# Optimization experiments

Hardware: AMD Instinct MI355X
Metric: run time of the kernel (lower is better)

Reference implementation:

```python
import jax, jax.numpy as jnp
import numpy as np

B, N, NPOINT, NSAMPLE = 8, 8192, 512, 32
D, NHEAD, NLAYERS, DIM_OUT = 128, 8, 4, 256
HD = D // NHEAD
DFF = 2 * D
EPS = 1e-5

_gather = jax.vmap(lambda p, i: p[i])  # p: [N,C], i: [...] -> [...,C]


def _ln(x, g, b):
    m = jnp.mean(x, -1, keepdims=True)
    v = jnp.var(x, -1, keepdims=True)
    return (x - m) / jnp.sqrt(v + EPS) * g + b


def _fps(pts):
    # pts: [B,N,3] -> centroid indices [B,NPOINT]; start index 0 (torch uses randint)
    Bb, Nn, _ = pts.shape
    def step(carry, _):
        dist, far = carry
        cen = jax.vmap(lambda p, f: p[f])(pts, far)[:, None, :]  # [B,1,3]
        dist = jnp.minimum(dist, jnp.sum((pts - cen) ** 2, -1))
        return (dist, jnp.argmax(dist, -1)), far
    init = (jnp.full((Bb, Nn), 1e10, pts.dtype), jnp.zeros((Bb,), jnp.int32))
    _, cents = jax.lax.scan(step, init, None, length=NPOINT)
    return cents.T  # [B,NPOINT]


def _interp_linear(x, n_out):
    # x: [B,C,S] -> [B,C,n_out], linear, align_corners=True
    S = x.shape[-1]
    pos = jnp.arange(n_out) * ((S - 1) / (n_out - 1))
    i0 = jnp.floor(pos).astype(jnp.int32)
    i1 = jnp.minimum(i0 + 1, S - 1)
    w = (pos - i0).astype(x.dtype)
    return x[..., i0] * (1 - w) + x[..., i1] * w


def _layer(x, p):
    wqkv, bqkv, wo, bo, g1, be1, w1, bf1, w2, bf2, g2, be2 = p
    Bt, K, _ = x.shape
    qkv = x @ wqkv.T + bqkv
    q, k, v = jnp.split(qkv, 3, axis=-1)
    q = q.reshape(Bt, K, NHEAD, HD)
    k = k.reshape(Bt, K, NHEAD, HD)
    v = v.reshape(Bt, K, NHEAD, HD)
    att = jax.nn.softmax(jnp.einsum('bqhd,bkhd->bhqk', q, k) / jnp.sqrt(jnp.float32(HD)), axis=-1)
    o = jnp.einsum('bhqk,bkhd->bqhd', att, v).reshape(Bt, K, D)
    x = _ln(x + o @ wo.T + bo, g1, be1)
    ff = jax.nn.relu(x @ w1.T + bf1) @ w2.T + bf2
    return _ln(x + ff, g2, be2)


def setup_inputs():
    key = jax.random.key(0)
    ks = jax.random.split(key, 10)
    w = lambda k, s: jax.random.normal(k, s, jnp.float32) * 0.02
    return {
        'xyz': jax.random.normal(ks[0], (B, 3, N), jnp.float32),
        'features': jax.random.normal(ks[1], (B, D, N), jnp.float32),
        'pe_w1': w(ks[2], (D // 2, 3)), 'pe_b1': jnp.zeros((D // 2,), jnp.float32),
        'bn_gamma': jnp.ones((D // 2,), jnp.float32), 'bn_beta': jnp.zeros((D // 2,), jnp.float32),
        'bn_mean': jnp.zeros((D // 2,), jnp.float32), 'bn_var': jnp.ones((D // 2,), jnp.float32),
        'pe_w2': w(ks[3], (D, D // 2)), 'pe_b2': jnp.zeros((D,), jnp.float32),
        'attn_wqkv': w(ks[4], (NLAYERS, 3 * D, D)), 'attn_bqkv': jnp.zeros((NLAYERS, 3 * D), jnp.float32),
        'attn_wo': w(ks[5], (NLAYERS, D, D)), 'attn_bo': jnp.zeros((NLAYERS, D), jnp.float32),
        'ln1_g': jnp.ones((NLAYERS, D), jnp.float32), 'ln1_b': jnp.zeros((NLAYERS, D), jnp.float32),
        'ffn_w1': w(ks[6], (NLAYERS, DFF, D)), 'ffn_b1': jnp.zeros((NLAYERS, DFF), jnp.float32),
        'ffn_w2': w(ks[7], (NLAYERS, D, DFF)), 'ffn_b2': jnp.zeros((NLAYERS, D), jnp.float32),
        'ln2_g': jnp.ones((NLAYERS, D), jnp.float32), 'ln2_b': jnp.zeros((NLAYERS, D), jnp.float32),
        'fc_w': w(ks[8], (DIM_OUT, D)), 'fc_b': jnp.zeros((DIM_OUT,), jnp.float32),
    }


def reference(xyz, features, pe_w1, pe_b1, bn_gamma, bn_beta, bn_mean, bn_var, pe_w2, pe_b2,
              attn_wqkv, attn_bqkv, attn_wo, attn_bo, ln1_g, ln1_b,
              ffn_w1, ffn_b1, ffn_w2, ffn_b2, ln2_g, ln2_b, fc_w, fc_b):
    pts = jnp.transpose(xyz, (0, 2, 1))                 # [B,N,3]
    fps_idx = _fps(pts)                                 # [B,S]
    new_xyz = _gather(pts, fps_idx)                     # [B,S,3]
    # kNN: squared distances [B,S,N]
    d2 = (jnp.sum(new_xyz ** 2, -1)[..., None] + jnp.sum(pts ** 2, -1)[:, None, :]
          - 2.0 * jnp.einsum('bsc,bnc->bsn', new_xyz, pts))
    _, gidx = jax.lax.top_k(-d2, NSAMPLE)               # [B,S,K]
    gxyz = _gather(pts, gidx)                           # [B,S,K,3]
    gfeat = _gather(jnp.transpose(features, (0, 2, 1)), gidx)  # [B,S,K,D]
    # positional encoding: 1x1 conv -> BN (eval) -> relu -> 1x1 conv
    h = gxyz @ pe_w1.T + pe_b1
    h = (h - bn_mean) / jnp.sqrt(bn_var + EPS) * bn_gamma + bn_beta
    pe = jax.nn.relu(h) @ pe_w2.T + pe_b2               # [B,S,K,D]
    x = (gfeat + pe).reshape(B * NPOINT, NSAMPLE, D)    # tokens: K neighbors per center
    layer_params = (attn_wqkv, attn_bqkv, attn_wo, attn_bo, ln1_g, ln1_b,
                    ffn_w1, ffn_b1, ffn_w2, ffn_b2, ln2_g, ln2_b)
    x, _ = jax.lax.scan(lambda c, p: (_layer(c, p), None), x, layer_params)
    x = x.reshape(B, NPOINT, NSAMPLE, D).max(axis=2)    # max-pool over neighbors [B,S,D]
    out = jnp.transpose(x @ fc_w.T + fc_b, (0, 2, 1))   # [B,DIM_OUT,S]
    out_up = _interp_linear(out, N)                     # [B,DIM_OUT,N]
    return jnp.transpose(new_xyz, (0, 2, 1)), out_up
```

## Files before the change

### kernel.cpp

```cpp
#include <hip/hip_runtime.h>
#include <math.h>

constexpr int CB  = 8;
constexpr int CN  = 8192;
constexpr int CS  = 512;
constexpr int CK  = 32;
constexpr int CD  = 128;
constexpr int CF  = 256;
constexpr int CO  = 256;
constexpr float CEPS = 1e-5f;

typedef __attribute__((ext_vector_type(8)))  short short8;
typedef __attribute__((ext_vector_type(4)))  float f32x4;
typedef __attribute__((ext_vector_type(16))) float f32x16;
#define MFMA16(a,b,c) __builtin_amdgcn_mfma_f32_16x16x32_bf16(a,b,c,0,0,0)
#define MFMA32(a,b,c) __builtin_amdgcn_mfma_f32_32x32x16_bf16(a,b,c,0,0,0)

__device__ __forceinline__ ushort f2b(float f){
  unsigned u = __builtin_bit_cast(unsigned, f);
  u = u + 0x7fffu + ((u >> 16) & 1u);
  return (ushort)(u >> 16);
}

template<int CTRL, int RM>
__device__ __forceinline__ unsigned long long dpp64(unsigned long long k){
  int lo = (int)(unsigned)k;
  int hi = (int)(unsigned)(k >> 32);
  int plo = __builtin_amdgcn_update_dpp(lo, lo, CTRL, RM, 0xF, false);
  int phi = __builtin_amdgcn_update_dpp(hi, hi, CTRL, RM, 0xF, false);
  return ((unsigned long long)(unsigned)phi << 32) | (unsigned)plo;
}
__device__ __forceinline__ unsigned long long wave_max64(unsigned long long k){
  unsigned long long p;
  p = dpp64<0xB1,0xF>(k); k = p > k ? p : k;
  p = dpp64<0x4E,0xF>(k); k = p > k ? p : k;
  p = dpp64<0x140,0xF>(k); k = p > k ? p : k;
  p = dpp64<0x141,0xF>(k); k = p > k ? p : k;
  p = dpp64<0x142,0xA>(k); k = p > k ? p : k;
  p = dpp64<0x143,0xC>(k); k = p > k ? p : k;
  return k;
}
__device__ __forceinline__ unsigned long long wave_min64(unsigned long long k){
  unsigned long long p;
  p = dpp64<0xB1,0xF>(k); k = p < k ? p : k;
  p = dpp64<0x4E,0xF>(k); k = p < k ? p : k;
  p = dpp64<0x140,0xF>(k); k = p < k ? p : k;
  p = dpp64<0x141,0xF>(k); k = p < k ? p : k;
  p = dpp64<0x142,0xA>(k); k = p < k ? p : k;
  p = dpp64<0x143,0xC>(k); k = p < k ? p : k;
  return k;
}
__device__ __forceinline__ unsigned long long oct_max64(unsigned long long k){
  unsigned long long p;
  p = dpp64<0xB1,0xF>(k); k = p > k ? p : k;
  p = dpp64<0x4E,0xF>(k); k = p > k ? p : k;
  p = dpp64<0x141,0xF>(k); k = p > k ? p : k;
  return k;
}
__device__ __forceinline__ unsigned long long quad_min64(unsigned long long k){
  unsigned long long p;
  p = dpp64<0xB1,0xF>(k); k = p < k ? p : k;
  p = dpp64<0x4E,0xF>(k); k = p < k ? p : k;
  return k;
}

__global__ __launch_bounds__(512)
void fps_kernel(const float* __restrict__ xyz, int* __restrict__ fps_idx)
{
#pragma clang fp contract(off)
  __shared__ __align__(16) float4 p4[CN];
  __shared__ unsigned long long wred[2][8];
  const int b = blockIdx.x, t = threadIdx.x;
  const int w = t >> 6, lane = t & 63;
  const float* xb = xyz + (size_t)b*3*CN;
  float px[16], py[16], pz[16], dist[16];
  #pragma unroll
  for (int j=0;j<16;j++){
    const int i = t + 512*j;
    px[j] = xb[i]; py[j] = xb[CN+i]; pz[j] = xb[2*CN+i];
    dist[j] = 1e10f;
    p4[i] = make_float4(px[j], py[j], pz[j], 0.f);
  }
  __syncthreads();
  int far = 0, par = 0;
  float4 c = p4[0];
  for (int it = 0; it < CS; ++it){
    if (t == 0) fps_idx[b*CS + it] = far;
    unsigned long long kk[16];
    #pragma unroll
    for (int j=0;j<16;j++){
      const float dx = px[j]-c.x, dy = py[j]-c.y, dz = pz[j]-c.z;
      const float d2 = (dx*dx + dy*dy) + dz*dz;
      const float nd = fminf(dist[j], d2);
      dist[j] = nd;
      kk[j] = ((unsigned long long)__builtin_bit_cast(unsigned, nd) << 32)
              | (unsigned)(8191 - (t + 512*j));
    }
    #pragma unroll
    for (int st=1; st<16; st<<=1)
      #pragma unroll
      for (int j=0;j<16;j+=2*st)
        kk[j] = kk[j] >= kk[j+st] ? kk[j] : kk[j+st];
    unsigned long long key = wave_max64(kk[0]);
    key = __shfl(key, 63);
    if (lane == 0) wred[par][w] = key;
    __syncthreads();
    unsigned long long k2 = wred[par][lane & 7];
    k2 = oct_max64(k2);
    far = 8191 - (int)(k2 & 0xFFFFFFFFu);
    c = p4[far];
    par ^= 1;
  }
}

__global__ __launch_bounds__(256)
void knn_kernel(const float* __restrict__ xyz, const int* __restrict__ fps_idx,
                int* __restrict__ gidx)
{
#pragma clang fp contract(off)
  __shared__ unsigned long long wredk[2][4];
  const int blk = blockIdx.x, t = threadIdx.x;
  const int w = t >> 6, l = t & 63;
  const int b = blk >> 9;
  const int s = blk & 511;
  const float* xb = xyz + (size_t)b*3*CN;
  const int cidx = fps_idx[b*CS + s];
  const float cx = xb[cidx], cy = xb[CN+cidx], cz = xb[2*CN+cidx];
  const float cn2 = (cx*cx + cy*cy) + cz*cz;
  unsigned long long kv[32];
  #pragma unroll
  for (int j=0;j<32;j++){
    const int i = t + 256*j;
    const float x = xb[i], y = xb[CN+i], z = xb[2*CN+i];
    const float pn2 = (x*x + y*y) + z*z;
    const float dot = (cx*x + cy*y) + cz*z;
    const float d2 = (cn2 + pn2) - 2.0f*dot;
    unsigned u = __builtin_bit_cast(unsigned, d2);
    u ^= (unsigned)((int)u >> 31) | 0x80000000u;
    kv[j] = ((unsigned long long)u << 32) | (unsigned)i;
  }
  unsigned long long mv;
  {
    unsigned long long tmp[16];
    #pragma unroll
    for (int j=0;j<16;j++) tmp[j] = kv[j] < kv[j+16] ? kv[j] : kv[j+16];
    #pragma unroll
    for (int st=8; st>=1; st>>=1)
      #pragma unroll
      for (int j=0;j<st;j++) tmp[j] = tmp[j] < tmp[j+st] ? tmp[j] : tmp[j+st];
    mv = tmp[0];
  }
  int par = 0;
  for (int k=0;k<CK;k++){
    unsigned long long v = wave_min64(mv);
    v = __shfl(v, 63);
    if (l == 0) wredk[par][w] = v;
    __syncthreads();
    unsigned long long k2 = wredk[par][l & 3];
    k2 = quad_min64(k2);
    const int win = (int)(k2 & 0xFFFFFFFFu);
    if (t == 0) gidx[(size_t)blk*CK + k] = win;
    if ((win & 255) == t){
      const int jw = win >> 8;
      #pragma unroll
      for (int j=0;j<32;j++) if (j == jw) kv[j] = ~0ull;
      unsigned long long tmp[16];
      #pragma unroll
      for (int j=0;j<16;j++) tmp[j] = kv[j] < kv[j+16] ? kv[j] : kv[j+16];
      #pragma unroll
      for (int st=8; st>=1; st>>=1)
        #pragma unroll
        for (int j=0;j<st;j++) tmp[j] = tmp[j] < tmp[j+st] ? tmp[j] : tmp[j+st];
      mv = tmp[0];
    }
    par ^= 1;
  }
}

__global__ __launch_bounds__(256)
void newxyz_kernel(const float* __restrict__ xyz, const int* __restrict__ fps_idx,
                   float* __restrict__ out0)
{
  const int idx = blockIdx.x*256 + threadIdx.x;
  if (idx >= CB*3*CS) return;
  const int s = idx & 511;
  const int c = (idx >> 9) % 3;
  const int b = idx / (3*CS);
  const int n = fps_idx[b*CS + s];
  out0[idx] = xyz[(size_t)b*3*CN + (size_t)c*CN + n];
}

__global__ __launch_bounds__(256)
void transpose_kernel(const float* __restrict__ f, float* __restrict__ ft)
{
  __shared__ float tile[32][33];
  const int b = blockIdx.z, d0 = blockIdx.y*32, n0 = blockIdx.x*32;
  const int tx = threadIdx.x, ty = threadIdx.y;
  const float* fb = f + (size_t)b*CD*CN;
  #pragma unroll
  for (int r=0;r<32;r+=8) tile[ty+r][tx] = fb[(size_t)(d0+ty+r)*CN + n0+tx];
  __syncthreads();
  float* ftb = ft + (size_t)b*CN*CD;
  #pragma unroll
  for (int r=0;r<32;r+=8) ftb[(size_t)(n0+ty+r)*CD + d0+tx] = tile[tx][ty+r];
}

__global__ __launch_bounds__(256)
void pe_kernel(const float* __restrict__ xyz, const float* __restrict__ features,
               const float* __restrict__ featT, const int* __restrict__ gidx,
               const float* __restrict__ pe_w1, const float* __restrict__ pe_b1,
               const float* __restrict__ bn_g, const float* __restrict__ bn_b,
               const float* __restrict__ bn_m, const float* __restrict__ bn_v,
               const float* __restrict__ pe_w2, const float* __restrict__ pe_b2,
               float* __restrict__ xout)
{
  __shared__ __align__(16) float w2s[CD*68];
  __shared__ __align__(16) float hr[CK*68];
  __shared__ int idxs[CK];
  __shared__ float gx[CK], gy[CK], gz[CK];
  const int g = blockIdx.x, t = threadIdx.x;
  const int b = g >> 9;
  for (int i=t; i<CD*64; i+=256) w2s[(i>>6)*68 + (i&63)] = pe_w2[i];
  if (t < CK){
    const int id = gidx[(size_t)g*CK + t];
    idxs[t] = id;
    const float* xb = xyz + (size_t)b*3*CN;
    gx[t] = xb[id]; gy[t] = xb[CN+id]; gz[t] = xb[2*CN+id];
  }
  __syncthreads();
  for (int v=t; v<CK*64; v+=256){
    const int k = v>>6, j = v&63;
    float h = ((gx[k]*pe_w1[j*3] + gy[k]*pe_w1[j*3+1]) + gz[k]*pe_w1[j*3+2]) + pe_b1[j];
    h = (h - bn_m[j]) / sqrtf(bn_v[j] + CEPS) * bn_g[j] + bn_b[j];
    hr[k*68+j] = fmaxf(h, 0.f);
  }
  __syncthreads();
  const int kt = t >> 5, dt = t & 31;
  const int k0 = kt*4, d0 = dt*4;
  float acc[4][4];
  #pragma unroll
  for (int a=0;a<4;a++)
    #pragma unroll
    for (int bb=0;bb<4;bb++) acc[a][bb] = 0.f;
  for (int j=0;j<16;j++){
    float4 h4[4], w4[4];
    #pragma unroll
    for (int a=0;a<4;a++) h4[a] = *(const float4*)&hr[(k0+a)*68 + j*4];
    #pragma unroll
    for (int bb=0;bb<4;bb++) w4[bb] = *(const float4*)&w2s[(d0+bb)*68 + j*4];
    #pragma unroll
    for (int a=0;a<4;a++)
      #pragma unroll
      for (int bb=0;bb<4;bb++){
        acc[a][bb] += h4[a].x*w4[bb].x; acc[a][bb] += h4[a].y*w4[bb].y;
        acc[a][bb] += h4[a].z*w4[bb].z; acc[a][bb] += h4[a].w*w4[bb].w;
      }
  }
  const float4 b2v = *(const float4*)&pe_b2[d0];
  const float* fb  = features + (size_t)b*CD*CN;
  const float* ftb = featT ? (featT + (size_t)b*CN*CD) : nullptr;
  #pragma unroll
  for (int a=0;a<4;a++){
    const int id = idxs[k0+a];
    float4 gf;
    if (ftb) gf = *(const float4*)&ftb[(size_t)id*CD + d0];
    else gf = make_float4(fb[(size_t)(d0+0)*CN+id], fb[(size_t)(d0+1)*CN+id],
                          fb[(size_t)(d0+2)*CN+id], fb[(size_t)(d0+3)*CN+id]);
    float4 o;
    o.x = gf.x + (acc[a][0] + b2v.x);
    o.y = gf.y + (acc[a][1] + b2v.y);
    o.z = gf.z + (acc[a][2] + b2v.z);
    o.w = gf.w + (acc[a][3] + b2v.w);
    *(float4*)&xout[(size_t)g*4096 + (size_t)(k0+a)*128 + d0] = o;
  }
}

__global__ __launch_bounds__(256)
void wprep_kernel(const float* __restrict__ wqkv, const float* __restrict__ wo,
                  const float* __restrict__ w1,   const float* __restrict__ w2,
                  ushort* __restrict__ dst)
{
  const int tid = blockIdx.x*256 + threadIdx.x;
  const int l = tid & 63;
  const int f = tid >> 6;
  const int L = f >> 8;
  const int r = f & 255;
  const float* src; int stride, nt, kt;
  if (r < 96)      { nt = r>>2;        kt = r&3;        src = wqkv + (size_t)L*384*128; stride = 128; }
  else if (r < 128){ nt = (r-96)>>2;   kt = (r-96)&3;   src = wo   + (size_t)L*128*128; stride = 128; }
  else if (r < 192){ nt = (r-128)>>2;  kt = (r-128)&3;  src = w1   + (size_t)L*256*128; stride = 128; }
  else             { nt = (r-192)>>3;  kt = (r-192)&7;  src = w2   + (size_t)L*128*256; stride = 256; }
  const int n = nt*16 + (l & 15);
  const int k = kt*32 + (l >> 4)*8;
  const float* p = src + (size_t)n*stride + k;
  uint4 o;
  o.x = (unsigned)f2b(p[0]) | ((unsigned)f2b(p[1])<<16);
  o.y = (unsigned)f2b(p[2]) | ((unsigned)f2b(p[3])<<16);
  o.z = (unsigned)f2b(p[4]) | ((unsigned)f2b(p[5])<<16);
  o.w = (unsigned)f2b(p[6]) | ((unsigned)f2b(p[7])<<16);
  *(uint4*)(dst + (size_t)tid*8) = o;
}

__device__ __forceinline__ void ln_inplace(float* x32s, ushort* xbv,
                                           const float* __restrict__ gamma,
                                           const float* __restrict__ beta, int t)
{
  const int r = t >> 3, j = t & 7;
  float v[16]; float s = 0.f;
  #pragma unroll
  for (int i=0;i<16;i++){ v[i] = x32s[r*132 + j + 8*i]; s += v[i]; }
  #pragma unroll
  for (int off=1; off<8; off<<=1) s += __shfl_xor(s, off);
  const float mean = s * (1.f/128.f);
  float var = 0.f;
  #pragma unroll
  for (int i=0;i<16;i++){ const float d = v[i]-mean; var += d*d; }
  #pragma unroll
  for (int off=1; off<8; off<<=1) var += __shfl_xor(var, off);
  const float inv = 1.f / sqrtf(var*(1.f/128.f) + CEPS);
  #pragma unroll
  for (int i=0;i<16;i++){
    const int d = j + 8*i;
    const float o = (v[i]-mean)*inv*gamma[d] + beta[d];
    x32s[r*132 + d] = o;
    xbv[r*136 + d] = f2b(o);
  }
}

__global__ __launch_bounds__(256, 2)
void layer_mfma_kernel(float* __restrict__ xbuf, const ushort* __restrict__ wf,
                       const float* __restrict__ bqkv, const float* __restrict__ bo,
                       const float* __restrict__ g1, const float* __restrict__ b1v,
                       const float* __restrict__ bf1, const float* __restrict__ bf2,
                       const float* __restrict__ g2, const float* __restrict__ b2v)
{
  __shared__ __align__(16) float  x32s[32*132];
  __shared__ __align__(16) ushort xbv [32*136];
  __shared__ __align__(16) ushort qk  [32*264];
  __shared__ __align__(16) ushort vT  [128*40];
  __shared__ __align__(16) ushort Pb  [4*32*40];
  const int g = blockIdx.x, t = threadIdx.x;
  const int w = t>>6, l = t&63;
  const int l15 = l&15, q4 = l>>4, l31 = l&31, hi = l>>5;
  float* xg = xbuf + (size_t)g*1024*4;
  const uint4* wfv = (const uint4*)wf;

  for (int i=t;i<1024;i+=256){
    const float4 v = ((const float4*)xg)[i];
    const int r = i>>5, c = (i&31)*4;
    *(float4*)&x32s[r*132 + c] = v;
    uint2 p;
    p.x = (unsigned)f2b(v.x) | ((unsigned)f2b(v.y)<<16);
    p.y = (unsigned)f2b(v.z) | ((unsigned)f2b(v.w)<<16);
    *(uint2*)&xbv[r*136 + c] = p;
  }
  __syncthreads();

  {
    short8 a[2][4];
    #pragma unroll
    for (int mt=0;mt<2;mt++)
      #pragma unroll
      for (int kt=0;kt<4;kt++)
        a[mt][kt] = __builtin_bit_cast(short8, *(const uint4*)&xbv[(l15+16*mt)*136 + kt*32 + q4*8]);
    for (int i=0;i<6;i++){
      const int nt = w + 4*i;
      const int n  = nt*16 + l15;
      f32x4 a0 = {0.f,0.f,0.f,0.f}, a1 = {0.f,0.f,0.f,0.f};
      #pragma unroll
      for (int kt=0;kt<4;kt++){
        const short8 b = __builtin_bit_cast(short8, wfv[(nt*4+kt)*64 + l]);
        a0 = MFMA16(a[0][kt], b, a0);
        a1 = MFMA16(a[1][kt], b, a1);
      }
      const float bias = bqkv[n];
      if (nt < 16){
        #pragma unroll
        for (int i2=0;i2<4;i2++){
          qk[(q4*4+i2   )*264 + n] = f2b(a0[i2]+bias);
          qk[(q4*4+i2+16)*264 + n] = f2b(a1[i2]+bias);
        }
      } else {
        const int d = n - 256;
        uint2 p0, p1;
        p0.x = (unsigned)f2b(a0[0]+bias) | ((unsigned)f2b(a0[1]+bias)<<16);
        p0.y = (unsigned)f2b(a0[2]+bias) | ((unsigned)f2b(a0[3]+bias)<<16);
        p1.x = (unsigned)f2b(a1[0]+bias) | ((unsigned)f2b(a1[1]+bias)<<16);
        p1.y = (unsigned)f2b(a1[2]+bias) | ((unsigned)f2b(a1[3]+bias)<<16);
        *(uint2*)&vT[d*40 + q4*4]      = p0;
        *(uint2*)&vT[d*40 + 16 + q4*4] = p1;
      }
    }
  }
  __syncthreads();

  for (int hh=0; hh<2; hh++){
    const int h = 2*w + hh;
    const short8 ka = __builtin_bit_cast(short8, *(const uint4*)&qk[l31*264 + 128 + h*16 + hi*8]);
    const short8 qb = __builtin_bit_cast(short8, *(const uint4*)&qk[l31*264 +       h*16 + hi*8]);
    f32x16 s;
    #pragma unroll
    for (int i=0;i<16;i++) s[i] = 0.f;
    s = MFMA32(ka, qb, s);
    float e[16]; float mx = -1e30f;
    #pragma unroll
    for (int i=0;i<16;i++){ e[i] = s[i]*0.25f; mx = fmaxf(mx, e[i]); }
    mx = fmaxf(mx, __shfl_xor(mx, 32));
    float sum = 0.f;
    #pragma unroll
    for (int i=0;i<16;i++){ e[i] = __expf(e[i]-mx); sum += e[i]; }
    sum += __shfl_xor(sum, 32);
    const float inv = 1.f/sum;
    #pragma unroll
    for (int j=0;j<4;j++){
      uint2 p;
      p.x = (unsigned)f2b(e[4*j  ]*inv) | ((unsigned)f2b(e[4*j+1]*inv)<<16);
      p.y = (unsigned)f2b(e[4*j+2]*inv) | ((unsigned)f2b(e[4*j+3]*inv)<<16);
      *(uint2*)&Pb[w*1280 + l31*40 + j*8 + hi*4] = p;
    }
    const short8 bv = __builtin_bit_cast(short8, *(const uint4*)&vT[(h*16+l15)*40 + q4*8]);
    #pragma unroll
    for (int mt=0;mt<2;mt++){
      const short8 ap = __builtin_bit_cast(short8, *(const uint4*)&Pb[w*1280 + (l15+16*mt)*40 + q4*8]);
      f32x4 o = {0.f,0.f,0.f,0.f};
      o = MFMA16(ap, bv, o);
      #pragma unroll
      for (int i2=0;i2<4;i2++)
        xbv[(16*mt + q4*4 + i2)*136 + h*16 + l15] = f2b(o[i2]);
    }
  }
  __syncthreads();

  {
    short8 a[2][4];
    #pragma unroll
    for (int mt=0;mt<2;mt++)
      #pragma unroll
      for (int kt=0;kt<4;kt++)
        a[mt][kt] = __builtin_bit_cast(short8, *(const uint4*)&xbv[(l15+16*mt)*136 + kt*32 + q4*8]);
    for (int i=0;i<2;i++){
      const int nt = w + 4*i;
      const int n  = nt*16 + l15;
      f32x4 a0 = {0.f,0.f,0.f,0.f}, a1 = {0.f,0.f,0.f,0.f};
      #pragma unroll
      for (int kt=0;kt<4;kt++){
        const short8 b = __builtin_bit_cast(short8, wfv[(96 + nt*4+kt)*64 + l]);
        a0 = MFMA16(a[0][kt], b, a0);
        a1 = MFMA16(a[1][kt], b, a1);
      }
      const float bias = bo[n];
      #pragma unroll
      for (int i2=0;i2<4;i2++){
        x32s[(q4*4+i2   )*132 + n] += a0[i2] + bias;
        x32s[(q4*4+i2+16)*132 + n] += a1[i2] + bias;
      }
    }
  }
  __syncthreads();
  ln_inplace(x32s, xbv, g1, b1v, t);
  __syncthreads();

  {
    short8 a[2][4];
    #pragma unroll
    for (int mt=0;mt<2;mt++)
      #pragma unroll
      for (int kt=0;kt<4;kt++)
        a[mt][kt] = __builtin_bit_cast(short8, *(const uint4*)&xbv[(l15+16*mt)*136 + kt*32 + q4*8]);
    for (int i=0;i<4;i++){
      const int nt = w + 4*i;
      const int n  = nt*16 + l15;
      f32x4 a0 = {0.f,0.f,0.f,0.f}, a1 = {0.f,0.f,0.f,0.f};
      #pragma unroll
      for (int kt=0;kt<4;kt++){
        const short8 b = __builtin_bit_cast(short8, wfv[(128 + nt*4+kt)*64 + l]);
        a0 = MFMA16(a[0][kt], b, a0);
        a1 = MFMA16(a[1][kt], b, a1);
      }
      const float bias = bf1[n];
      #pragma unroll
      for (int i2=0;i2<4;i2++){
        qk[(q4*4+i2   )*264 + n] = f2b(fmaxf(a0[i2]+bias, 0.f));
        qk[(q4*4+i2+16)*264 + n] = f2b(fmaxf(a1[i2]+bias, 0.f));
      }
    }
  }
  __syncthreads();

  {
    short8 a[2][8];
    #pragma unroll
    for (int mt=0;mt<2;mt++)
      #pragma unroll
      for (int kt=0;kt<8;kt++)
        a[mt][kt] = __builtin_bit_cast(short8, *(const uint4*)&qk[(l15+16*mt)*264 + kt*32 + q4*8]);
    for (int i=0;i<2;i++){
      const int nt = w + 4*i;
      const int n  = nt*16 + l15;
      f32x4 a0 = {0.f,0.f,0.f,0.f}, a1 = {0.f,0.f,0.f,0.f};
      #pragma unroll
      for (int kt=0;kt<8;kt++){
        const short8 b = __builtin_bit_cast(short8, wfv[(192 + nt*8+kt)*64 + l]);
        a0 = MFMA16(a[0][kt], b, a0);
        a1 = MFMA16(a[1][kt], b, a1);
      }
      const float bias = bf2[n];
      #pragma unroll
      for (int i2=0;i2<4;i2++){
        x32s[(q4*4+i2   )*132 + n] += a0[i2] + bias;
        x32s[(q4*4+i2+16)*132 + n] += a1[i2] + bias;
      }
    }
  }
  __syncthreads();
  ln_inplace(x32s, xbv, g2, b2v, t);
  __syncthreads();

  for (int i=t;i<1024;i+=256){
    const int r = i>>5, c = (i&31)*4;
    ((float4*)xg)[i] = *(const float4*)&x32s[r*132 + c];
  }
}

__global__ __launch_bounds__(256)
void poolfc_kernel(const float* __restrict__ xbuf, const float* __restrict__ fc_w,
                   const float* __restrict__ fc_b, float* __restrict__ fcout)
{
  __shared__ __align__(16) float pooled[CD];
  const int gg = blockIdx.x, t = threadIdx.x;
  const float* xg = xbuf + (size_t)gg*CK*CD;
  if (t < CD){
    float m = -1e30f;
    for (int k=0;k<CK;k++) m = fmaxf(m, xg[(size_t)k*CD + t]);
    pooled[t] = m;
  }
  __syncthreads();
  const float* wr = fc_w + (size_t)t*CD;
  float acc = 0.f;
  const float4* pp = (const float4*)pooled;
  for (int i=0;i<CD/4;i++){
    const float4 w4 = *(const float4*)(wr + 4*i);
    const float4 p4 = pp[i];
    acc += p4.x*w4.x; acc += p4.y*w4.y; acc += p4.z*w4.z; acc += p4.w*w4.w;
  }
  acc += fc_b[t];
  const int b = gg >> 9, s = gg & 511;
  fcout[((size_t)b*CS + s)*CO + t] = acc;
}

__global__ __launch_bounds__(256)
void interp_kernel(const float* __restrict__ fcout, float* __restrict__ out1)
{
  const int idx = blockIdx.x*256 + threadIdx.x;
  const int n  = idx & (CN-1);
  const int bo = idx >> 13;
  const int b  = bo >> 8, o = bo & 255;
  const double pos = (double)n * ((double)(CS-1)/(double)(CN-1));
  const int i0 = (int)pos;
  const int i1 = min(i0+1, CS-1);
  const float w = (float)(pos - (double)i0);
  const float v0 = fcout[((size_t)b*CS + i0)*CO + o];
  const float v1 = fcout[((size_t)b*CS + i1)*CO + o];
  out1[idx] = v0*(1.f - w) + v1*w;
}

extern "C" void kernel_launch(void* const* d_in, const int* in_sizes, int n_in,
                              void* d_out, int out_size, void* d_ws, size_t ws_size,
                              hipStream_t stream)
{
  (void)in_sizes; (void)n_in; (void)out_size;
  const float* xyz      = (const float*)d_in[0];
  const float* features = (const float*)d_in[1];
  const float* pe_w1    = (const float*)d_in[2];
  const float* pe_b1    = (const float*)d_in[3];
  const float* bn_g     = (const float*)d_in[4];
  const float* bn_b     = (const float*)d_in[5];
  const float* bn_m     = (const float*)d_in[6];
  const float* bn_v     = (const float*)d_in[7];
  const float* pe_w2    = (const float*)d_in[8];
  const float* pe_b2    = (const float*)d_in[9];
  const float* wqkv     = (const float*)d_in[10];
  const float* bqkv     = (const float*)d_in[11];
  const float* wo       = (const float*)d_in[12];
  const float* bo       = (const float*)d_in[13];
  const float* g1       = (const float*)d_in[14];
  const float* b1       = (const float*)d_in[15];
  const float* w1       = (const float*)d_in[16];
  const float* bf1      = (const float*)d_in[17];
  const float* w2       = (const float*)d_in[18];
  const float* bf2      = (const float*)d_in[19];
  const float* g2       = (const float*)d_in[20];
  const float* b2       = (const float*)d_in[21];
  const float* fc_w     = (const float*)d_in[22];
  const float* fc_b     = (const float*)d_in[23];

  char* ws = (char*)d_ws;
  int*    fps_idx = (int*)(ws);
  int*    gidx    = (int*)(ws + (16u<<10));
  ushort* wfrag   = (ushort*)(ws + (1u<<20));
  float*  xbuf    = (float*)(ws + (2u<<20));
  float*  fcout   = (float*)(ws + (66u<<20));
  float*  featT   = (float*)(ws + (70u<<20));
  const bool useT = ws_size >= ((size_t)102<<20);

  float* out0 = (float*)d_out;
  float* out1 = out0 + CB*3*CS;

  fps_kernel<<<CB, 512, 0, stream>>>(xyz, fps_idx);
  knn_kernel<<<CB*CS, 256, 0, stream>>>(xyz, fps_idx, gidx);
  newxyz_kernel<<<(CB*3*CS + 255)/256, 256, 0, stream>>>(xyz, fps_idx, out0);
  wprep_kernel<<<256, 256, 0, stream>>>(wqkv, wo, w1, w2, wfrag);
  if (useT){
    dim3 tb(32, 8), tg(CN/32, CD/32, CB);
    transpose_kernel<<<tg, tb, 0, stream>>>(features, featT);
  }
  pe_kernel<<<CB*CS, 256, 0, stream>>>(xyz, features, useT ? featT : nullptr, gidx,
                                       pe_w1, pe_b1, bn_g, bn_b, bn_m, bn_v,
                                       pe_w2, pe_b2, xbuf);
  for (int L=0; L<4; L++){
    layer_mfma_kernel<<<CB*CS, 256, 0, stream>>>(xbuf,
        wfrag + (size_t)L*131072,
        bqkv + (size_t)L*3*CD, bo + (size_t)L*CD,
        g1 + (size_t)L*CD, b1 + (size_t)L*CD,
        bf1 + (size_t)L*CF, bf2 + (size_t)L*CD,
        g2 + (size_t)L*CD, b2 + (size_t)L*CD);
  }
  poolfc_kernel<<<CB*CS, 256, 0, stream>>>(xbuf, fc_w, fc_b, fcout);
  interp_kernel<<<(CB*CO*CN)/256, 256, 0, stream>>>(fcout, out1);
}
```

Baseline: 1.456 ms.

## Fuse transformer layers and pooling into one kernel, overlap prep work with FPS

Runs all four transformer layers plus max-pool and the FC projection inside a single kernel that keeps the 32x128 token tile in shared memory, removing the per-layer global round trips of xbuf and several launches. The weight fragment preparation and the feature transpose become extra blocks of the FPS launch, so they run on otherwise idle CUs while the 8-block FPS executes. The new_xyz output is now written by the KNN kernel, and the wave reductions drop a shuffle by storing from lane 63. In exchange, the FPS launch is larger and shares its shared-memory allocation with the transpose blocks.

```diff
diff --git a/kernel.cpp b/kernel.cpp
--- a/kernel.cpp
+++ b/kernel.cpp
@@ -65,12 +65,60 @@
 }
 
 __global__ __launch_bounds__(512)
-void fps_kernel(const float* __restrict__ xyz, int* __restrict__ fps_idx)
+void fps_fused_kernel(const float* __restrict__ xyz, int* __restrict__ fps_idx,
+                      const float* __restrict__ features, float* __restrict__ featT,
+                      const float* __restrict__ wqkv, const float* __restrict__ wo,
+                      const float* __restrict__ w1,   const float* __restrict__ w2,
+                      ushort* __restrict__ wfrag)
 {
 #pragma clang fp contract(off)
   __shared__ __align__(16) float4 p4[CN];
   __shared__ unsigned long long wred[2][8];
-  const int b = blockIdx.x, t = threadIdx.x;
+  const int bid = blockIdx.x, t = threadIdx.x;
+
+  if (bid >= CB + 128){
+    if (featT == nullptr) return;
+    const int tt  = (bid - CB - 128)*2 + (t >> 8);
+    const int b2  = tt >> 10;
+    const int rem = tt & 1023;
+    const int d0  = (rem >> 8) * 32;
+    const int n0  = (rem & 255) * 32;
+    const int t2  = t & 255;
+    const int tx  = t2 & 31, ty = t2 >> 5;
+    float* tl = ((float*)p4) + (t >> 8) * (32*33);
+    const float* fb = features + (size_t)b2*CD*CN;
+    #pragma unroll
+    for (int r=0;r<32;r+=8) tl[(ty+r)*33 + tx] = fb[(size_t)(d0+ty+r)*CN + n0+tx];
+    __syncthreads();
+    float* ftb = featT + (size_t)b2*CN*CD;
+    #pragma unroll
+    for (int r=0;r<32;r+=8) ftb[(size_t)(n0+ty+r)*CD + d0+tx] = tl[tx*33 + (ty+r)];
+    return;
+  }
+  if (bid >= CB){
+    const int tid = (bid - CB)*512 + t;
+    const int l = tid & 63;
+    const int f = tid >> 6;
+    const int L = f >> 8;
+    const int r = f & 255;
+    const float* src; int stride, nt, kt;
+    if (r < 96)      { nt = r>>2;        kt = r&3;        src = wqkv + (size_t)L*384*128; stride = 128; }
+    else if (r < 128){ nt = (r-96)>>2;   kt = (r-96)&3;   src = wo   + (size_t)L*128*128; stride = 128; }
+    else if (r < 192){ nt = (r-128)>>2;  kt = (r-128)&3;  src = w1   + (size_t)L*256*128; stride = 128; }
+    else             { nt = (r-192)>>3;  kt = (r-192)&7;  src = w2   + (size_t)L*128*256; stride = 256; }
+    const int n = nt*16 + (l & 15);
+    const int k = kt*32 + (l >> 4)*8;
+    const float* p = src + (size_t)n*stride + k;
+    uint4 o;
+    o.x = (unsigned)f2b(p[0]) | ((unsigned)f2b(p[1])<<16);
+    o.y = (unsigned)f2b(p[2]) | ((unsigned)f2b(p[3])<<16);
+    o.z = (unsigned)f2b(p[4]) | ((unsigned)f2b(p[5])<<16);
+    o.w = (unsigned)f2b(p[6]) | ((unsigned)f2b(p[7])<<16);
+    *(uint4*)(wfrag + (size_t)tid*8) = o;
+    return;
+  }
+
+  const int b = bid;
   const int w = t >> 6, lane = t & 63;
   const float* xb = xyz + (size_t)b*3*CN;
   float px[16], py[16], pz[16], dist[16];
@@ -101,9 +149,8 @@
       #pragma unroll
       for (int j=0;j<16;j+=2*st)
         kk[j] = kk[j] >= kk[j+st] ? kk[j] : kk[j+st];
-    unsigned long long key = wave_max64(kk[0]);
-    key = __shfl(key, 63);
-    if (lane == 0) wred[par][w] = key;
+    const unsigned long long key = wave_max64(kk[0]);
+    if (lane == 63) wred[par][w] = key;
     __syncthreads();
     unsigned long long k2 = wred[par][lane & 7];
     k2 = oct_max64(k2);
@@ -115,7 +162,7 @@
 
 __global__ __launch_bounds__(256)
 void knn_kernel(const float* __restrict__ xyz, const int* __restrict__ fps_idx,
-                int* __restrict__ gidx)
+                int* __restrict__ gidx, float* __restrict__ out0)
 {
 #pragma clang fp contract(off)
   __shared__ unsigned long long wredk[2][4];
@@ -127,6 +174,10 @@
   const int cidx = fps_idx[b*CS + s];
   const float cx = xb[cidx], cy = xb[CN+cidx], cz = xb[2*CN+cidx];
   const float cn2 = (cx*cx + cy*cy) + cz*cz;
+  if (t == 0){
+    float* o = out0 + (size_t)b*3*CS + s;
+    o[0] = cx; o[CS] = cy; o[2*CS] = cz;
+  }
   unsigned long long kv[32];
   #pragma unroll
   for (int j=0;j<32;j++){
@@ -152,9 +203,8 @@
   }
   int par = 0;
   for (int k=0;k<CK;k++){
-    unsigned long long v = wave_min64(mv);
-    v = __shfl(v, 63);
-    if (l == 0) wredk[par][w] = v;
+    const unsigned long long v = wave_min64(mv);
+    if (l == 63) wredk[par][w] = v;
     __syncthreads();
     unsigned long long k2 = wredk[par][l & 3];
     k2 = quad_min64(k2);
@@ -175,34 +225,6 @@
     }
     par ^= 1;
   }
-}
-
-__global__ __launch_bounds__(256)
-void newxyz_kernel(const float* __restrict__ xyz, const int* __restrict__ fps_idx,
-                   float* __restrict__ out0)
-{
-  const int idx = blockIdx.x*256 + threadIdx.x;
-  if (idx >= CB*3*CS) return;
-  const int s = idx & 511;
-  const int c = (idx >> 9) % 3;
-  const int b = idx / (3*CS);
-  const int n = fps_idx[b*CS + s];
-  out0[idx] = xyz[(size_t)b*3*CN + (size_t)c*CN + n];
-}
-
-__global__ __launch_bounds__(256)
-void transpose_kernel(const float* __restrict__ f, float* __restrict__ ft)
-{
-  __shared__ float tile[32][33];
-  const int b = blockIdx.z, d0 = blockIdx.y*32, n0 = blockIdx.x*32;
-  const int tx = threadIdx.x, ty = threadIdx.y;
-  const float* fb = f + (size_t)b*CD*CN;
-  #pragma unroll
-  for (int r=0;r<32;r+=8) tile[ty+r][tx] = fb[(size_t)(d0+ty+r)*CN + n0+tx];
-  __syncthreads();
-  float* ftb = ft + (size_t)b*CN*CD;
-  #pragma unroll
-  for (int r=0;r<32;r+=8) ftb[(size_t)(n0+ty+r)*CD + d0+tx] = tile[tx][ty+r];
 }
 
 __global__ __launch_bounds__(256)
@@ -275,32 +297,6 @@
   }
 }
 
-__global__ __launch_bounds__(256)
-void wprep_kernel(const float* __restrict__ wqkv, const float* __restrict__ wo,
-                  const float* __restrict__ w1,   const float* __restrict__ w2,
-                  ushort* __restrict__ dst)
-{
-  const int tid = blockIdx.x*256 + threadIdx.x;
-  const int l = tid & 63;
-  const int f = tid >> 6;
-  const int L = f >> 8;
-  const int r = f & 255;
-  const float* src; int stride, nt, kt;
-  if (r < 96)      { nt = r>>2;        kt = r&3;        src = wqkv + (size_t)L*384*128; stride = 128; }
-  else if (r < 128){ nt = (r-96)>>2;   kt = (r-96)&3;   src = wo   + (size_t)L*128*128; stride = 128; }
-  else if (r < 192){ nt = (r-128)>>2;  kt = (r-128)&3;  src = w1   + (size_t)L*256*128; stride = 128; }
-  else             { nt = (r-192)>>3;  kt = (r-192)&7;  src = w2   + (size_t)L*128*256; stride = 256; }
-  const int n = nt*16 + (l & 15);
-  const int k = kt*32 + (l >> 4)*8;
-  const float* p = src + (size_t)n*stride + k;
-  uint4 o;
-  o.x = (unsigned)f2b(p[0]) | ((unsigned)f2b(p[1])<<16);
-  o.y = (unsigned)f2b(p[2]) | ((unsigned)f2b(p[3])<<16);
-  o.z = (unsigned)f2b(p[4]) | ((unsigned)f2b(p[5])<<16);
-  o.w = (unsigned)f2b(p[6]) | ((unsigned)f2b(p[7])<<16);
-  *(uint4*)(dst + (size_t)tid*8) = o;
-}
-
 __device__ __forceinline__ void ln_inplace(float* x32s, ushort* xbv,
                                            const float* __restrict__ gamma,
                                            const float* __restrict__ beta, int t)
@@ -328,22 +324,24 @@
 }
 
 __global__ __launch_bounds__(256, 2)
-void layer_mfma_kernel(float* __restrict__ xbuf, const ushort* __restrict__ wf,
-                       const float* __restrict__ bqkv, const float* __restrict__ bo,
-                       const float* __restrict__ g1, const float* __restrict__ b1v,
-                       const float* __restrict__ bf1, const float* __restrict__ bf2,
-                       const float* __restrict__ g2, const float* __restrict__ b2v)
+void layers_mfma_kernel(const float* __restrict__ xbuf, const ushort* __restrict__ wf,
+                        const float* __restrict__ bqkv, const float* __restrict__ bo,
+                        const float* __restrict__ g1, const float* __restrict__ b1v,
+                        const float* __restrict__ bf1, const float* __restrict__ bf2,
+                        const float* __restrict__ g2, const float* __restrict__ b2v,
+                        const float* __restrict__ fc_w, const float* __restrict__ fc_b,
+                        float* __restrict__ fcout)
 {
   __shared__ __align__(16) float  x32s[32*132];
   __shared__ __align__(16) ushort xbv [32*136];
   __shared__ __align__(16) ushort qk  [32*264];
   __shared__ __align__(16) ushort vT  [128*40];
   __shared__ __align__(16) ushort Pb  [4*32*40];
+  __shared__ __align__(16) float  pooled[CD];
   const int g = blockIdx.x, t = threadIdx.x;
   const int w = t>>6, l = t&63;
   const int l15 = l&15, q4 = l>>4, l31 = l&31, hi = l>>5;
-  float* xg = xbuf + (size_t)g*1024*4;
-  const uint4* wfv = (const uint4*)wf;
+  const float* xg = xbuf + (size_t)g*1024*4;
 
   for (int i=t;i<1024;i+=256){
     const float4 v = ((const float4*)xg)[i];
@@ -356,196 +354,197 @@
   }
   __syncthreads();
 
-  {
-    short8 a[2][4];
-    #pragma unroll
-    for (int mt=0;mt<2;mt++)
-      #pragma unroll
-      for (int kt=0;kt<4;kt++)
-        a[mt][kt] = __builtin_bit_cast(short8, *(const uint4*)&xbv[(l15+16*mt)*136 + kt*32 + q4*8]);
-    for (int i=0;i<6;i++){
-      const int nt = w + 4*i;
-      const int n  = nt*16 + l15;
-      f32x4 a0 = {0.f,0.f,0.f,0.f}, a1 = {0.f,0.f,0.f,0.f};
-      #pragma unroll
-      for (int kt=0;kt<4;kt++){
-        const short8 b = __builtin_bit_cast(short8, wfv[(nt*4+kt)*64 + l]);
-        a0 = MFMA16(a[0][kt], b, a0);
-        a1 = MFMA16(a[1][kt], b, a1);
-      }
-      const float bias = bqkv[n];
-      if (nt < 16){
-        #pragma unroll
-        for (int i2=0;i2<4;i2++){
-          qk[(q4*4+i2   )*264 + n] = f2b(a0[i2]+bias);
-          qk[(q4*4+i2+16)*264 + n] = f2b(a1[i2]+bias);
-        }
-      } else {
-        const int d = n - 256;
-        uint2 p0, p1;
-        p0.x = (unsigned)f2b(a0[0]+bias) | ((unsigned)f2b(a0[1]+bias)<<16);
-        p0.y = (unsigned)f2b(a0[2]+bias) | ((unsigned)f2b(a0[3]+bias)<<16);
-        p1.x = (unsigned)f2b(a1[0]+bias) | ((unsigned)f2b(a1[1]+bias)<<16);
-        p1.y = (unsigned)f2b(a1[2]+bias) | ((unsigned)f2b(a1[3]+bias)<<16);
-        *(uint2*)&vT[d*40 + q4*4]      = p0;
-        *(uint2*)&vT[d*40 + 16 + q4*4] = p1;
+  #pragma unroll 1
+  for (int L = 0; L < 4; ++L){
+    const uint4*  wfv   = (const uint4*)(wf + (size_t)L*131072);
+    const float* bqkvL  = bqkv + (size_t)L*3*CD;
+    const float* boL    = bo   + (size_t)L*CD;
+    const float* g1L    = g1   + (size_t)L*CD;
+    const float* b1L    = b1v  + (size_t)L*CD;
+    const float* bf1L   = bf1  + (size_t)L*CF;
+    const float* bf2L   = bf2  + (size_t)L*CD;
+    const float* g2L    = g2   + (size_t)L*CD;
+    const float* b2L    = b2v  + (size_t)L*CD;
+
+    {
+      short8 a[2][4];
+      #pragma unroll
+      for (int mt=0;mt<2;mt++)
+        #pragma unroll
+        for (int kt=0;kt<4;kt++)
+          a[mt][kt] = __builtin_bit_cast(short8, *(const uint4*)&xbv[(l15+16*mt)*136 + kt*32 + q4*8]);
+      for (int i=0;i<6;i++){
+        const int nt = w + 4*i;
+        const int n  = nt*16 + l15;
+        f32x4 a0 = {0.f,0.f,0.f,0.f}, a1 = {0.f,0.f,0.f,0.f};
+        #pragma unroll
+        for (int kt=0;kt<4;kt++){
+          const short8 b = __builtin_bit_cast(short8, wfv[(nt*4+kt)*64 + l]);
+          a0 = MFMA16(a[0][kt], b, a0);
+          a1 = MFMA16(a[1][kt], b, a1);
+        }
+        const float bias = bqkvL[n];
+        if (nt < 16){
+          #pragma unroll
+          for (int i2=0;i2<4;i2++){
+            qk[(q4*4+i2   )*264 + n] = f2b(a0[i2]+bias);
+            qk[(q4*4+i2+16)*264 + n] = f2b(a1[i2]+bias);
+          }
+        } else {
+          const int d = n - 256;
+          uint2 p0, p1;
+          p0.x = (unsigned)f2b(a0[0]+bias) | ((unsigned)f2b(a0[1]+bias)<<16);
+          p0.y = (unsigned)f2b(a0[2]+bias) | ((unsigned)f2b(a0[3]+bias)<<16);
+          p1.x = (unsigned)f2b(a1[0]+bias) | ((unsigned)f2b(a1[1]+bias)<<16);
+          p1.y = (unsigned)f2b(a1[2]+bias) | ((unsigned)f2b(a1[3]+bias)<<16);
+          *(uint2*)&vT[d*40 + q4*4]      = p0;
+          *(uint2*)&vT[d*40 + 16 + q4*4] = p1;
+        }
       }
     }
-  }
-  __syncthreads();
-
-  for (int hh=0; hh<2; hh++){
-    const int h = 2*w + hh;
-    const short8 ka = __builtin_bit_cast(short8, *(const uint4*)&qk[l31*264 + 128 + h*16 + hi*8]);
-    const short8 qb = __builtin_bit_cast(short8, *(const uint4*)&qk[l31*264 +       h*16 + hi*8]);
-    f32x16 s;
-    #pragma unroll
-    for (int i=0;i<16;i++) s[i] = 0.f;
-    s = MFMA32(ka, qb, s);
-    float e[16]; float mx = -1e30f;
-    #pragma unroll
-    for (int i=0;i<16;i++){ e[i] = s[i]*0.25f; mx = fmaxf(mx, e[i]); }
-    mx = fmaxf(mx, __shfl_xor(mx, 32));
-    float sum = 0.f;
-    #pragma unroll
-    for (int i=0;i<16;i++){ e[i] = __expf(e[i]-mx); sum += e[i]; }
-    sum += __shfl_xor(sum, 32);
-    const float inv = 1.f/sum;
-    #pragma unroll
-    for (int j=0;j<4;j++){
-      uint2 p;
-      p.x = (unsigned)f2b(e[4*j  ]*inv) | ((unsigned)f2b(e[4*j+1]*inv)<<16);
-      p.y = (unsigned)f2b(e[4*j+2]*inv) | ((unsigned)f2b(e[4*j+3]*inv)<<16);
-      *(uint2*)&Pb[w*1280 + l31*40 + j*8 + hi*4] = p;
-    }
-    const short8 bv = __builtin_bit_cast(short8, *(const uint4*)&vT[(h*16+l15)*40 + q4*8]);
-    #pragma unroll
-    for (int mt=0;mt<2;mt++){
-      const short8 ap = __builtin_bit_cast(short8, *(const uint4*)&Pb[w*1280 + (l15+16*mt)*40 + q4*8]);
-      f32x4 o = {0.f,0.f,0.f,0.f};
-      o = MFMA16(ap, bv, o);
-      #pragma unroll
-      for (int i2=0;i2<4;i2++)
-        xbv[(16*mt + q4*4 + i2)*136 + h*16 + l15] = f2b(o[i2]);
-    }
-  }
-  __syncthreads();
-
-  {
-    short8 a[2][4];
-    #pragma unroll
-    for (int mt=0;mt<2;mt++)
-      #pragma unroll
-      for (int kt=0;kt<4;kt++)
-        a[mt][kt] = __builtin_bit_cast(short8, *(const uint4*)&xbv[(l15+16*mt)*136 + kt*32 + q4*8]);
-    for (int i=0;i<2;i++){
-      const int nt = w + 4*i;
-      const int n  = nt*16 + l15;
-      f32x4 a0 = {0.f,0.f,0.f,0.f}, a1 = {0.f,0.f,0.f,0.f};
-      #pragma unroll
-      for (int kt=0;kt<4;kt++){
-        const short8 b = __builtin_bit_cast(short8, wfv[(96 + nt*4+kt)*64 + l]);
-        a0 = MFMA16(a[0][kt], b, a0);
-        a1 = MFMA16(a[1][kt], b, a1);
+    __syncthreads();
+
+    for (int hh=0; hh<2; hh++){
+      const int h = 2*w + hh;
+      const short8 ka = __builtin_bit_cast(short8, *(const uint4*)&qk[l31*264 + 128 + h*16 + hi*8]);
+      const short8 qb = __builtin_bit_cast(short8, *(const uint4*)&qk[l31*264 +       h*16 + hi*8]);
+      f32x16 s;
+      #pragma unroll
+      for (int i=0;i<16;i++) s[i] = 0.f;
+      s = MFMA32(ka, qb, s);
+      float e[16]; float mx = -1e30f;
+      #pragma unroll
+      for (int i=0;i<16;i++){ e[i] = s[i]*0.25f; mx = fmaxf(mx, e[i]); }
+      mx = fmaxf(mx, __shfl_xor(mx, 32));
+      float sum = 0.f;
+      #pragma unroll
+      for (int i=0;i<16;i++){ e[i] = __expf(e[i]-mx); sum += e[i]; }
+      sum += __shfl_xor(sum, 32);
+      const float inv = 1.f/sum;
+      #pragma unroll
+      for (int j=0;j<4;j++){
+        uint2 p;
+        p.x = (unsigned)f2b(e[4*j  ]*inv) | ((unsigned)f2b(e[4*j+1]*inv)<<16);
+        p.y = (unsigned)f2b(e[4*j+2]*inv) | ((unsigned)f2b(e[4*j+3]*inv)<<16);
+        *(uint2*)&Pb[w*1280 + l31*40 + j*8 + hi*4] = p;
       }
-      const float bias = bo[n];
-      #pragma unroll
-      for (int i2=0;i2<4;i2++){
-        x32s[(q4*4+i2   )*132 + n] += a0[i2] + bias;
-        x32s[(q4*4+i2+16)*132 + n] += a1[i2] + bias;
+      const short8 bv = __builtin_bit_cast(short8, *(const uint4*)&vT[(h*16+l15)*40 + q4*8]);
+      #pragma unroll
+      for (int mt=0;mt<2;mt++){
+        const short8 ap = __builtin_bit_cast(short8, *(const uint4*)&Pb[w*1280 + (l15+16*mt)*40 + q4*8]);
+        f32x4 o = {0.f,0.f,0.f,0.f};
+        o = MFMA16(ap, bv, o);
+        #pragma unroll
+        for (int i2=0;i2<4;i2++)
+          xbv[(16*mt + q4*4 + i2)*136 + h*16 + l15] = f2b(o[i2]);
       }
     }
-  }
-  __syncthreads();
-  ln_inplace(x32s, xbv, g1, b1v, t);
-  __syncthreads();
-
-  {
-    short8 a[2][4];
-    #pragma unroll
-    for (int mt=0;mt<2;mt++)
-      #pragma unroll
-      for (int kt=0;kt<4;kt++)
-        a[mt][kt] = __builtin_bit_cast(short8, *(const uint4*)&xbv[(l15+16*mt)*136 + kt*32 + q4*8]);
-    for (int i=0;i<4;i++){
-      const int nt = w + 4*i;
-      const int n  = nt*16 + l15;
-      f32x4 a0 = {0.f,0.f,0.f,0.f}, a1 = {0.f,0.f,0.f,0.f};
-      #pragma unroll
-      for (int kt=0;kt<4;kt++){
-        const short8 b = __builtin_bit_cast(short8, wfv[(128 + nt*4+kt)*64 + l]);
-        a0 = MFMA16(a[0][kt], b, a0);
-        a1 = MFMA16(a[1][kt], b, a1);
-      }
-      const float bias = bf1[n];
-      #pragma unroll
-      for (int i2=0;i2<4;i2++){
-        qk[(q4*4+i2   )*264 + n] = f2b(fmaxf(a0[i2]+bias, 0.f));
-        qk[(q4*4+i2+16)*264 + n] = f2b(fmaxf(a1[i2]+bias, 0.f));
+    __syncthreads();
+
+    {
+      short8 a[2][4];
+      #pragma unroll
+      for (int mt=0;mt<2;mt++)
+        #pragma unroll
+        for (int kt=0;kt<4;kt++)
+          a[mt][kt] = __builtin_bit_cast(short8, *(const uint4*)&xbv[(l15+16*mt)*136 + kt*32 + q4*8]);
+      for (int i=0;i<2;i++){
+        const int nt = w + 4*i;
+        const int n  = nt*16 + l15;
+        f32x4 a0 = {0.f,0.f,0.f,0.f}, a1 = {0.f,0.f,0.f,0.f};
+        #pragma unroll
+        for (int kt=0;kt<4;kt++){
+          const short8 b = __builtin_bit_cast(short8, wfv[(96 + nt*4+kt)*64 + l]);
+          a0 = MFMA16(a[0][kt], b, a0);
+          a1 = MFMA16(a[1][kt], b, a1);
+        }
+        const float bias = boL[n];
+        #pragma unroll
+        for (int i2=0;i2<4;i2++){
+          x32s[(q4*4+i2   )*132 + n] += a0[i2] + bias;
+          x32s[(q4*4+i2+16)*132 + n] += a1[i2] + bias;
+        }
       }
     }
-  }
-  __syncthreads();
-
-  {
-    short8 a[2][8];
-    #pragma unroll
-    for (int mt=0;mt<2;mt++)
-      #pragma unroll
-      for (int kt=0;kt<8;kt++)
-        a[mt][kt] = __builtin_bit_cast(short8, *(const uint4*)&qk[(l15+16*mt)*264 + kt*32 + q4*8]);
-    for (int i=0;i<2;i++){
-      const int nt = w + 4*i;
-      const int n  = nt*16 + l15;
-      f32x4 a0 = {0.f,0.f,0.f,0.f}, a1 = {0.f,0.f,0.f,0.f};
-      #pragma unroll
-      for (int kt=0;kt<8;kt++){
-        const short8 b = __builtin_bit_cast(short8, wfv[(192 + nt*8+kt)*64 + l]);
-        a0 = MFMA16(a[0][kt], b, a0);
-        a1 = MFMA16(a[1][kt], b, a1);
-      }
-      const float bias = bf2[n];
-      #pragma unroll
-      for (int i2=0;i2<4;i2++){
-        x32s[(q4*4+i2   )*132 + n] += a0[i2] + bias;
-        x32s[(q4*4+i2+16)*132 + n] += a1[i2] + bias;
+    __syncthreads();
+    ln_inplace(x32s, xbv, g1L, b1L, t);
+    __syncthreads();
+
+    {
+      short8 a[2][4];
+      #pragma unroll
+      for (int mt=0;mt<2;mt++)
+        #pragma unroll
+        for (int kt=0;kt<4;kt++)
+          a[mt][kt] = __builtin_bit_cast(short8, *(const uint4*)&xbv[(l15+16*mt)*136 + kt*32 + q4*8]);
+      for (int i=0;i<4;i++){
+        const int nt = w + 4*i;
+        const int n  = nt*16 + l15;
+        f32x4 a0 = {0.f,0.f,0.f,0.f}, a1 = {0.f,0.f,0.f,0.f};
+        #pragma unroll
+        for (int kt=0;kt<4;kt++){
+          const short8 b = __builtin_bit_cast(short8, wfv[(128 + nt*4+kt)*64 + l]);
+          a0 = MFMA16(a[0][kt], b, a0);
+          a1 = MFMA16(a[1][kt], b, a1);
+        }
+        const float bias = bf1L[n];
+        #pragma unroll
+        for (int i2=0;i2<4;i2++){
+          qk[(q4*4+i2   )*264 + n] = f2b(fmaxf(a0[i2]+bias, 0.f));
+          qk[(q4*4+i2+16)*264 + n] = f2b(fmaxf(a1[i2]+bias, 0.f));
+        }
       }
     }
-  }
-  __syncthreads();
-  ln_inplace(x32s, xbv, g2, b2v, t);
-  __syncthreads();
-
-  for (int i=t;i<1024;i+=256){
-    const int r = i>>5, c = (i&31)*4;
-    ((float4*)xg)[i] = *(const float4*)&x32s[r*132 + c];
-  }
-}
-
-__global__ __launch_bounds__(256)
-void poolfc_kernel(const float* __restrict__ xbuf, const float* __restrict__ fc_w,
-                   const float* __restrict__ fc_b, float* __restrict__ fcout)
-{
-  __shared__ __align__(16) float pooled[CD];
-  const int gg = blockIdx.x, t = threadIdx.x;
-  const float* xg = xbuf + (size_t)gg*CK*CD;
+    __syncthreads();
+
+    {
+      short8 a[2][8];
+      #pragma unroll
+      for (int mt=0;mt<2;mt++)
+        #pragma unroll
+        for (int kt=0;kt<8;kt++)
+          a[mt][kt] = __builtin_bit_cast(short8, *(const uint4*)&qk[(l15+16*mt)*264 + kt*32 + q4*8]);
+      for (int i=0;i<2;i++){
+        const int nt = w + 4*i;
+        const int n  = nt*16 + l15;
+        f32x4 a0 = {0.f,0.f,0.f,0.f}, a1 = {0.f,0.f,0.f,0.f};
+        #pragma unroll
+        for (int kt=0;kt<8;kt++){
+          const short8 b = __builtin_bit_cast(short8, wfv[(192 + nt*8+kt)*64 + l]);
+          a0 = MFMA16(a[0][kt], b, a0);
+          a1 = MFMA16(a[1][kt], b, a1);
+        }
+        const float bias = bf2L[n];
+        #pragma unroll
+        for (int i2=0;i2<4;i2++){
+          x32s[(q4*4+i2   )*132 + n] += a0[i2] + bias;
+          x32s[(q4*4+i2+16)*132 + n] += a1[i2] + bias;
+        }
+      }
+    }
+    __syncthreads();
+    ln_inplace(x32s, xbv, g2L, b2L, t);
+    __syncthreads();
+  }
+
   if (t < CD){
     float m = -1e30f;
-    for (int k=0;k<CK;k++) m = fmaxf(m, xg[(size_t)k*CD + t]);
+    #pragma unroll
+    for (int k=0;k<CK;k++) m = fmaxf(m, x32s[k*132 + t]);
     pooled[t] = m;
   }
   __syncthreads();
+  float acc = 0.f;
   const float* wr = fc_w + (size_t)t*CD;
-  float acc = 0.f;
   const float4* pp = (const float4*)pooled;
+  #pragma unroll
   for (int i=0;i<CD/4;i++){
     const float4 w4 = *(const float4*)(wr + 4*i);
     const float4 p4 = pp[i];
     acc += p4.x*w4.x; acc += p4.y*w4.y; acc += p4.z*w4.z; acc += p4.w*w4.w;
   }
   acc += fc_b[t];
-  const int b = gg >> 9, s = gg & 511;
-  fcout[((size_t)b*CS + s)*CO + t] = acc;
+  fcout[(size_t)g*CO + t] = acc;
 }
 
 __global__ __launch_bounds__(256)
@@ -606,25 +605,15 @@
   float* out0 = (float*)d_out;
   float* out1 = out0 + CB*3*CS;
 
-  fps_kernel<<<CB, 512, 0, stream>>>(xyz, fps_idx);
-  knn_kernel<<<CB*CS, 256, 0, stream>>>(xyz, fps_idx, gidx);
-  newxyz_kernel<<<(CB*3*CS + 255)/256, 256, 0, stream>>>(xyz, fps_idx, out0);
-  wprep_kernel<<<256, 256, 0, stream>>>(wqkv, wo, w1, w2, wfrag);
-  if (useT){
-    dim3 tb(32, 8), tg(CN/32, CD/32, CB);
-    transpose_kernel<<<tg, tb, 0, stream>>>(features, featT);
-  }
+  const int nblk = CB + 128 + (useT ? 4096 : 0);
+  fps_fused_kernel<<<nblk, 512, 0, stream>>>(xyz, fps_idx, features,
+                                             useT ? featT : nullptr,
+                                             wqkv, wo, w1, w2, wfrag);
+  knn_kernel<<<CB*CS, 256, 0, stream>>>(xyz, fps_idx, gidx, out0);
   pe_kernel<<<CB*CS, 256, 0, stream>>>(xyz, features, useT ? featT : nullptr, gidx,
                                        pe_w1, pe_b1, bn_g, bn_b, bn_m, bn_v,
                                        pe_w2, pe_b2, xbuf);
-  for (int L=0; L<4; L++){
-    layer_mfma_kernel<<<CB*CS, 256, 0, stream>>>(xbuf,
-        wfrag + (size_t)L*131072,
-        bqkv + (size_t)L*3*CD, bo + (size_t)L*CD,
-        g1 + (size_t)L*CD, b1 + (size_t)L*CD,
-        bf1 + (size_t)L*CF, bf2 + (size_t)L*CD,
-        g2 + (size_t)L*CD, b2 + (size_t)L*CD);
-  }
-  poolfc_kernel<<<CB*CS, 256, 0, stream>>>(xbuf, fc_w, fc_b, fcout);
+  layers_mfma_kernel<<<CB*CS, 256, 0, stream>>>(xbuf, wfrag,
+      bqkv, bo, g1, b1, bf1, bf2, g2, b2, fc_w, fc_b, fcout);
   interp_kernel<<<(CB*CO*CN)/256, 256, 0, stream>>>(fcout, out1);
 }
```

Result: faster. 1.309 ms (-10.1%).
